# Kernel tuning notes

Hardware: AMD Instinct MI355X
Metric: run time of the kernel (lower is better)

## Reference

```python
import jax, jax.numpy as jnp
import numpy as np

B, N, C, H, P, L = 32, 64, 8, 64, 16, 8  # batch, nodes, commodities, hidden, max_paths, max_path_len


def setup_inputs() -> dict:
    key = jax.random.key(0)
    ks = jax.random.split(key, 8)
    edge_features = jax.random.normal(ks[0], (B, N, N, C, H), dtype=jnp.float32)
    graph_embedding = jax.random.normal(ks[1], (B, H), dtype=jnp.float32)
    selected_commodity = jax.random.randint(ks[2], (B,), 0, C, dtype=jnp.int32)
    paths = jax.random.randint(ks[3], (B, P, L), 0, N, dtype=jnp.int32)
    path_len = jnp.clip(jax.random.randint(ks[4], (B, P), 0, 9), 2, L).astype(jnp.int32)
    path_mask = jnp.ones((B, P), dtype=bool)
    W1 = jax.random.normal(ks[5], (2 * H, 128), dtype=jnp.float32) * (1.0 / np.sqrt(2 * H))
    b1 = jnp.zeros((128,), dtype=jnp.float32)
    W2 = jax.random.normal(ks[6], (128, 1), dtype=jnp.float32) * (1.0 / np.sqrt(128))
    b2 = jnp.zeros((1,), dtype=jnp.float32)
    return {"edge_features": edge_features, "graph_embedding": graph_embedding,
            "selected_commodity": selected_commodity, "paths": paths,
            "path_len": path_len, "path_mask": path_mask,
            "W1": W1, "b1": b1, "W2": W2, "b2": b2}


def reference(edge_features, graph_embedding, selected_commodity, paths, path_len,
              path_mask, W1, b1, W2, b2):
    # per-path edges (u, v): [B, P, E] with E = L - 1
    u = paths[:, :, :-1]
    v = paths[:, :, 1:]
    E = u.shape[2]
    b_idx = jnp.arange(B)[:, None, None]
    c_idx = selected_commodity[:, None, None]
    # gather edge features along each path: [B, P, E, H]
    feats = edge_features[b_idx, u, v, c_idx]
    # valid-edge mask from path lengths (paths with len<2 -> zero feature)
    emask = (jnp.arange(E)[None, None, :] < (path_len[:, :, None] - 1)).astype(feats.dtype)
    cnt = emask.sum(axis=2, keepdims=True)  # [B, P, 1]
    path_feat = (feats * emask[..., None]).sum(axis=2) / jnp.maximum(cnt, 1.0)  # [B, P, H]
    g = jnp.broadcast_to(graph_embedding[:, None, :], path_feat.shape)
    inp = jnp.concatenate([path_feat, g], axis=-1)  # [B, P, 2H]
    h = jax.nn.relu(inp @ W1 + b1)
    scores = (h @ W2 + b2)[..., 0]  # [B, P]
    neg_inf = jnp.asarray(-jnp.inf, scores.dtype)
    scores = jnp.where(path_mask, scores, neg_inf)
    action_probs = jax.nn.softmax(scores, axis=-1)
    log_probs = jax.nn.log_softmax(scores, axis=-1)
    log_probs_safe = jnp.where(path_mask, log_probs, 0.0)
    entropy = -(action_probs * log_probs_safe).sum(axis=-1)
    return (action_probs, log_probs, entropy)
```

## Files before the change

kernel.cpp:

```cpp
#include <hip/hip_runtime.h>
#include <math.h>

#define BB 32
#define NN 64
#define CC 8
#define HH 64
#define PP 16
#define LL 8

__global__ __launch_bounds__(1024) void path_selector_kernel(
    const float* __restrict__ ef,
    const float* __restrict__ ge,
    const int*   __restrict__ sc,
    const int*   __restrict__ paths,
    const int*   __restrict__ plen,
    const int*   __restrict__ pmask,
    const float* __restrict__ W1,
    const float* __restrict__ b1,
    const float* __restrict__ W2,
    const float* __restrict__ b2,
    float* __restrict__ out)
{
    __shared__ float s_g[HH];
    __shared__ float s_pf[PP][HH];
    __shared__ float s_score[PP];

    const int b    = blockIdx.x;
    const int tid  = threadIdx.x;
    const int wave = tid >> 6;
    const int lane = tid & 63;
    const int p    = wave;

    const int c = sc[b];

    if (tid < HH) s_g[tid] = ge[b * HH + tid];

    {
        const int* pp = paths + (b * PP + p) * LL;
        int cnt = plen[b * PP + p] - 1;
        cnt = (cnt < 1) ? 1 : (cnt > LL - 1 ? LL - 1 : cnt);
        int node[LL];
        #pragma unroll
        for (int l = 0; l < LL; ++l) node[l] = pp[l];
        float s = 0.0f;
        for (int e = 0; e < cnt; ++e) {
            int u = node[e];
            int v = node[e + 1];
            int idx = (((b * NN + u) * NN + v) * CC + c) * HH + lane;
            s += ef[idx];
        }
        s_pf[p][lane] = s / (float)cnt;
    }
    __syncthreads();

    {
        float h1 = b1[lane];
        float h2 = b1[64 + lane];
        const float* pf = s_pf[p];
        #pragma unroll 8
        for (int k = 0; k < 64; ++k) {
            float a = pf[k];
            h1 += a * W1[k * 128 + lane];
            h2 += a * W1[k * 128 + 64 + lane];
        }
        #pragma unroll 8
        for (int k = 0; k < 64; ++k) {
            float a = s_g[k];
            h1 += a * W1[(64 + k) * 128 + lane];
            h2 += a * W1[(64 + k) * 128 + 64 + lane];
        }
        h1 = fmaxf(h1, 0.0f);
        h2 = fmaxf(h2, 0.0f);
        float cs = h1 * W2[lane] + h2 * W2[64 + lane];
        #pragma unroll
        for (int off = 32; off >= 1; off >>= 1)
            cs += __shfl_down(cs, off, 64);
        if (lane == 0) s_score[p] = cs + b2[0];
    }
    __syncthreads();

    if (wave == 0 && lane < PP) {
        const bool m = pmask[b * PP + lane] != 0;
        const float s = m ? s_score[lane] : -INFINITY;

        float mx = s;
        #pragma unroll
        for (int off = 8; off >= 1; off >>= 1)
            mx = fmaxf(mx, __shfl_xor(mx, off, 64));

        const float e = m ? expf(s - mx) : 0.0f;
        float se = e;
        #pragma unroll
        for (int off = 8; off >= 1; off >>= 1)
            se += __shfl_xor(se, off, 64);

        const float prob = e / se;
        const float lse  = logf(se);
        const float lp   = (s - mx) - lse;
        const float lps  = m ? lp : 0.0f;

        float ent = -prob * lps;
        #pragma unroll
        for (int off = 8; off >= 1; off >>= 1)
            ent += __shfl_xor(ent, off, 64);

        out[b * PP + lane]            = prob;
        out[BB * PP + b * PP + lane]  = lp;
        if (lane == 0) out[2 * BB * PP + b] = ent;
    }
}

extern "C" void kernel_launch(void* const* d_in, const int* in_sizes, int n_in,
                              void* d_out, int out_size, void* d_ws, size_t ws_size,
                              hipStream_t stream) {
    const float* ef    = (const float*)d_in[0];
    const float* ge    = (const float*)d_in[1];
    const int*   sc    = (const int*)d_in[2];
    const int*   paths = (const int*)d_in[3];
    const int*   plen  = (const int*)d_in[4];
    const int*   pmask = (const int*)d_in[5];
    const float* W1    = (const float*)d_in[6];
    const float* b1    = (const float*)d_in[7];
    const float* W2    = (const float*)d_in[8];
    const float* b2    = (const float*)d_in[9];
    float*       out   = (float*)d_out;

    path_selector_kernel<<<BB, PP * 64, 0, stream>>>(
        ef, ge, sc, paths, plen, pmask, W1, b1, W2, b2, out);
}
```

Before: 317.1 us.

## Split path scoring and softmax into two kernels with more, smaller blocks

Splits the fused kernel into two. The first launches 128 blocks of 4 waves, one wave per (batch, path), to compute the MLP scores. It broadcasts the path feature and graph embedding through wave shuffles instead of shared memory and writes scores to workspace. The second kernel does the masked softmax, log-softmax and entropy per batch. The aim is to spread the work across more compute units than 32 large blocks allow, at the cost of an extra launch and a global round-trip for the scores.

```diff
diff --git a/kernel.cpp b/kernel.cpp
--- a/kernel.cpp
+++ b/kernel.cpp
@@ -8,106 +8,100 @@
 #define PP 16
 #define LL 8
 
-__global__ __launch_bounds__(1024) void path_selector_kernel(
+__global__ __launch_bounds__(256) void score_kernel(
     const float* __restrict__ ef,
     const float* __restrict__ ge,
     const int*   __restrict__ sc,
     const int*   __restrict__ paths,
     const int*   __restrict__ plen,
-    const int*   __restrict__ pmask,
     const float* __restrict__ W1,
     const float* __restrict__ b1,
     const float* __restrict__ W2,
     const float* __restrict__ b2,
-    float* __restrict__ out)
+    float* __restrict__ scores)
 {
-    __shared__ float s_g[HH];
-    __shared__ float s_pf[PP][HH];
-    __shared__ float s_score[PP];
-
-    const int b    = blockIdx.x;
-    const int tid  = threadIdx.x;
-    const int wave = tid >> 6;
-    const int lane = tid & 63;
-    const int p    = wave;
+    const int gw   = (blockIdx.x * blockDim.x + threadIdx.x) >> 6;
+    const int lane = threadIdx.x & 63;
+    const int b    = gw >> 4;
+    const int p    = gw & 15;
 
     const int c = sc[b];
 
-    if (tid < HH) s_g[tid] = ge[b * HH + tid];
+    const int* pp = paths + (b * PP + p) * LL;
+    int cnt = plen[b * PP + p] - 1;
+    cnt = (cnt < 1) ? 1 : (cnt > LL - 1 ? LL - 1 : cnt);
+    int node[LL];
+    #pragma unroll
+    for (int l = 0; l < LL; ++l) node[l] = pp[l];
+    float s = 0.0f;
+    for (int e = 0; e < cnt; ++e) {
+        int u = node[e];
+        int v = node[e + 1];
+        int idx = (((b * NN + u) * NN + v) * CC + c) * HH + lane;
+        s += ef[idx];
+    }
+    const float pf = s / (float)cnt;
+    const float gv = ge[b * HH + lane];
 
-    {
-        const int* pp = paths + (b * PP + p) * LL;
-        int cnt = plen[b * PP + p] - 1;
-        cnt = (cnt < 1) ? 1 : (cnt > LL - 1 ? LL - 1 : cnt);
-        int node[LL];
-        #pragma unroll
-        for (int l = 0; l < LL; ++l) node[l] = pp[l];
-        float s = 0.0f;
-        for (int e = 0; e < cnt; ++e) {
-            int u = node[e];
-            int v = node[e + 1];
-            int idx = (((b * NN + u) * NN + v) * CC + c) * HH + lane;
-            s += ef[idx];
-        }
-        s_pf[p][lane] = s / (float)cnt;
+    float h1 = b1[lane];
+    float h2 = b1[64 + lane];
+    #pragma unroll 8
+    for (int k = 0; k < 64; ++k) {
+        float a = __shfl(pf, k, 64);
+        h1 += a * W1[k * 128 + lane];
+        h2 += a * W1[k * 128 + 64 + lane];
     }
-    __syncthreads();
+    #pragma unroll 8
+    for (int k = 0; k < 64; ++k) {
+        float a = __shfl(gv, k, 64);
+        h1 += a * W1[(64 + k) * 128 + lane];
+        h2 += a * W1[(64 + k) * 128 + 64 + lane];
+    }
+    h1 = fmaxf(h1, 0.0f);
+    h2 = fmaxf(h2, 0.0f);
+    float cs = h1 * W2[lane] + h2 * W2[64 + lane];
+    #pragma unroll
+    for (int off = 32; off >= 1; off >>= 1)
+        cs += __shfl_down(cs, off, 64);
+    if (lane == 0) scores[b * PP + p] = cs + b2[0];
+}
 
-    {
-        float h1 = b1[lane];
-        float h2 = b1[64 + lane];
-        const float* pf = s_pf[p];
-        #pragma unroll 8
-        for (int k = 0; k < 64; ++k) {
-            float a = pf[k];
-            h1 += a * W1[k * 128 + lane];
-            h2 += a * W1[k * 128 + 64 + lane];
-        }
-        #pragma unroll 8
-        for (int k = 0; k < 64; ++k) {
-            float a = s_g[k];
-            h1 += a * W1[(64 + k) * 128 + lane];
-            h2 += a * W1[(64 + k) * 128 + 64 + lane];
-        }
-        h1 = fmaxf(h1, 0.0f);
-        h2 = fmaxf(h2, 0.0f);
-        float cs = h1 * W2[lane] + h2 * W2[64 + lane];
-        #pragma unroll
-        for (int off = 32; off >= 1; off >>= 1)
-            cs += __shfl_down(cs, off, 64);
-        if (lane == 0) s_score[p] = cs + b2[0];
-    }
-    __syncthreads();
+__global__ __launch_bounds__(64) void softmax_kernel(
+    const float* __restrict__ scores,
+    const int*   __restrict__ pmask,
+    float* __restrict__ out)
+{
+    const int b    = blockIdx.x;
+    const int lane = threadIdx.x & 63;
+    if (lane >= PP) return;
 
-    if (wave == 0 && lane < PP) {
-        const bool m = pmask[b * PP + lane] != 0;
-        const float s = m ? s_score[lane] : -INFINITY;
+    const bool m = pmask[b * PP + lane] != 0;
+    const float s = m ? scores[b * PP + lane] : -INFINITY;
 
-        float mx = s;
-        #pragma unroll
-        for (int off = 8; off >= 1; off >>= 1)
-            mx = fmaxf(mx, __shfl_xor(mx, off, 64));
+    float mx = s;
+    #pragma unroll
+    for (int off = 8; off >= 1; off >>= 1)
+        mx = fmaxf(mx, __shfl_xor(mx, off, 64));
 
-        const float e = m ? expf(s - mx) : 0.0f;
-        float se = e;
-        #pragma unroll
-        for (int off = 8; off >= 1; off >>= 1)
-            se += __shfl_xor(se, off, 64);
+    const float e = m ? expf(s - mx) : 0.0f;
+    float se = e;
+    #pragma unroll
+    for (int off = 8; off >= 1; off >>= 1)
+        se += __shfl_xor(se, off, 64);
 
-        const float prob = e / se;
-        const float lse  = logf(se);
-        const float lp   = (s - mx) - lse;
-        const float lps  = m ? lp : 0.0f;
+    const float prob = e / se;
+    const float lse  = logf(se);
+    const float lp   = (s - mx) - lse;
+    const float lps  = m ? lp : 0.0f;
 
-        float ent = -prob * lps;
-        #pragma unroll
-        for (int off = 8; off >= 1; off >>= 1)
-            ent += __shfl_xor(ent, off, 64);
+    float ent = -prob * lps;
+    #pragma unroll
+    for (int off = 8; off >= 1; off >>= 1)
+        ent += __shfl_xor(ent, off, 64);
 
-        out[b * PP + lane]            = prob;
-        out[BB * PP + b * PP + lane]  = lp;
-        if (lane == 0) out[2 * BB * PP + b] = ent;
-    }
+    out[b * PP + lane]           = prob;
+    out[BB * PP + b * PP + lane] = lp;
+    if (lane == 0) out[2 * BB * PP + b] = ent;
 }
 
 extern "C" void kernel_launch(void* const* d_in, const int* in_sizes, int n_in,
@@ -124,7 +118,9 @@
     const float* W2    = (const float*)d_in[8];
     const float* b2    = (const float*)d_in[9];
     float*       out   = (float*)d_out;
+    float*       scores = (float*)d_ws;
 
-    path_selector_kernel<<<BB, PP * 64, 0, stream>>>(
-        ef, ge, sc, paths, plen, pmask, W1, b1, W2, b2, out);
+    score_kernel<<<(BB * PP) / 4, 256, 0, stream>>>(
+        ef, ge, sc, paths, plen, W1, b1, W2, b2, scores);
+    softmax_kernel<<<BB, 64, 0, stream>>>(scores, pmask, out);
 }
```

Result: no change. 314.8 us (-0.7%).
